# Optimization experiments

Hardware: AMD Instinct MI355X
Metric: run time of the kernel (lower is better)

Reference implementation:

```python
import jax, jax.numpy as jnp
import numpy as np

NUM_FRAMES = 32
H, W = 1024, 1024
MAX_DEPTH = 5
PROB_THRESHOLD = 1e-3  # torch skips children with topk prob <= 0.001


def setup_inputs() -> dict:
    key = jax.random.key(0)
    k1, k2 = jax.random.split(key)
    frame_colors = jax.random.uniform(k1, (NUM_FRAMES, 3), dtype=jnp.float32)
    # torch init: rand(num_frames, 2, num_frames) * 5
    frame_selection = jax.random.uniform(k2, (NUM_FRAMES, 2, NUM_FRAMES), dtype=jnp.float32) * 5.0
    return {"frame_colors": frame_colors, "frame_selection": frame_selection, "temperature": 1}


def _np_softmax(x):
    e = np.exp(x - x.max(axis=-1, keepdims=True))
    return e / e.sum(axis=-1, keepdims=True)


def _render(idx, depth, h, w, fc, fs_probs, probs_np, memo):
    # Output depends only on (idx, depth, h, w) since split_ratio is a constant
    # 0.5 buffer and split_direction = idx % 2, so identical subtrees are memoized.
    key = (idx, depth, h, w)
    if key in memo:
        return memo[key]
    if depth >= MAX_DEPTH or w < 2 or h < 2:
        out = jnp.broadcast_to(jax.nn.sigmoid(fc[idx]).reshape(3, 1, 1), (3, h, w))
    else:
        vertical = (idx % 2) == 1  # split_directions[i] = i % 2
        if vertical:
            lw = max(1, int(w * 0.5))
            child_sizes = ((h, lw), (h, w - lw))  # left cols [0:lw], right cols [lw:]
        else:
            th = max(1, int(h * 0.5))
            child_sizes = ((th, w), (h - th, w))  # top rows [0:th], bottom rows [th:]
        k = 3 if depth < 2 else (2 if depth < 4 else 1)
        k = min(k, NUM_FRAMES)
        parts = []
        for side in range(2):  # 0 = left/top, 1 = right/bottom
            ch, cw = child_sizes[side]
            pn = probs_np[idx, side]
            order = np.argsort(-pn)[:k]  # top-k child frame indices (constant w.r.t. grads)
            probs = fs_probs[idx, side]
            acc = jnp.zeros((3, ch, cw), dtype=fc.dtype)
            for i in order:
                if pn[i] > PROB_THRESHOLD:  # same skip rule as torch, decided on concrete values
                    child = _render(int(i), depth + 1, ch, cw, fc, fs_probs, probs_np, memo)
                    acc = acc + probs[i] * child
            parts.append(acc)
        out = jnp.concatenate(parts, axis=2 if vertical else 1)
    memo[key] = out
    return out


def reference(frame_colors, frame_selection, temperature):
    t = float(temperature)
    fs_probs = jax.nn.softmax(frame_selection / t, axis=-1)  # (F, 2, F) differentiable weights
    probs_np = _np_softmax(np.asarray(frame_selection, dtype=np.float64) / t)  # structure only
    return _render(0, 0, H, W, frame_colors, fs_probs, probs_np, {})
```

## Files before the change

### kernel.cpp

```cpp
#include <hip/hip_runtime.h>
#include <math.h>

#define NF 32
#define HH 1024
#define WW 1024

__device__ __forceinline__ int descend(int idx, int py, int px,
                                       int& y0, int& x0, int& h, int& w) {
  int side;
  if (idx & 1) {
    int lw = w >> 1;
    if (px >= x0 + lw) { side = 1; x0 += lw; w -= lw; }
    else               { side = 0; w = lw; }
  } else {
    int th = h >> 1;
    if (py >= y0 + th) { side = 1; y0 += th; h -= th; }
    else               { side = 0; h = th; }
  }
  return side;
}

__global__ __launch_bounds__(256)
void fractal_kernel(const float* __restrict__ fc,
                    const float* __restrict__ fsel,
                    const int* __restrict__ temp,
                    float* __restrict__ out) {
  __shared__ float sProbs[64][33];
  __shared__ int   sOrder[64][3];
  __shared__ float sSig[NF][3];
  __shared__ float sCol[3];

  const int tid  = threadIdx.x;
  const int tile = blockIdx.x;
  const int by = tile >> 5, bx = tile & 31;
  const int py = by * 32 + 16, px = bx * 32 + 16;

  int   ti = temp[0];
  float t  = (ti > 0 && ti < 1000000) ? (float)ti : __int_as_float(ti);
  const float invT = 1.0f / t;

  for (int v = 0; v < 8; ++v) {
    int u = v * 256 + tid;
    sProbs[u >> 5][u & 31] = fsel[u] * invT;
  }
  if (tid >= 64 && tid < 160) {
    int j = tid - 64;
    sSig[j / 3][j % 3] = 1.0f / (1.0f + expf(-fc[j]));
  }
  __syncthreads();

  if (tid < 64) {
    float m = -1e30f;
    for (int i = 0; i < 32; ++i) m = fmaxf(m, sProbs[tid][i]);
    float s = 0.f;
    for (int i = 0; i < 32; ++i) {
      float e = expf(sProbs[tid][i] - m);
      sProbs[tid][i] = e;
      s += e;
    }
    float inv = 1.0f / s;
    float v0 = -1.f, v1 = -1.f, v2 = -1.f;
    int   b0 = 0,    b1 = 0,    b2 = 0;
    for (int i = 0; i < 32; ++i) {
      float p = sProbs[tid][i] * inv;
      sProbs[tid][i] = p;
      if (p > v0)      { v2=v1;b2=b1; v1=v0;b1=b0; v0=p;b0=i; }
      else if (p > v1) { v2=v1;b2=b1; v1=p;b1=i; }
      else if (p > v2) { v2=p;b2=i; }
    }
    sOrder[tid][0] = b0; sOrder[tid][1] = b1; sOrder[tid][2] = b2;
  }
  __syncthreads();

  if (tid < 64) {
    float c0 = 0.f, c1 = 0.f, c2 = 0.f;
    if (tid < 36) {
      int j = tid;
      int sel0 = j / 12; int r = j % 12;
      int sel1 = r / 4;  r &= 3;
      int sel2 = r >> 1;
      int sel3 = r & 1;
      int selArr[5] = { sel0, sel1, sel2, sel3, 0 };

      int idx = 0, ay = 0, ax = 0, ah = HH, aw = WW;
      float w = 1.0f;
      bool alive = true;
      for (int d = 0; d < 5; ++d) {
        int s   = descend(idx, py, px, ay, ax, ah, aw);
        int row = idx * 2 + s;
        int ci  = sOrder[row][selArr[d]];
        float p = sProbs[row][ci];
        if (p <= 1e-3f) { alive = false; break; }
        w  *= p;
        idx = ci;
      }
      if (alive) {
        c0 = w * sSig[idx][0];
        c1 = w * sSig[idx][1];
        c2 = w * sSig[idx][2];
      }
    }
    for (int off = 32; off > 0; off >>= 1) {
      c0 += __shfl_down(c0, off, 64);
      c1 += __shfl_down(c1, off, 64);
      c2 += __shfl_down(c2, off, 64);
    }
    if (tid == 0) { sCol[0] = c0; sCol[1] = c1; sCol[2] = c2; }
  }
  __syncthreads();

  const int r = tid >> 3;
  const int q = tid & 7;
  for (int c = 0; c < 3; ++c) {
    float v = sCol[c];
    float4 val = make_float4(v, v, v, v);
    float* base = out + (size_t)c * (HH * WW)
                      + (size_t)(by * 32 + r) * WW + (size_t)bx * 32;
    ((float4*)base)[q] = val;
  }
}

extern "C" void kernel_launch(void* const* d_in, const int* in_sizes, int n_in,
                              void* d_out, int out_size, void* d_ws, size_t ws_size,
                              hipStream_t stream) {
  const float* fc   = (const float*)d_in[0];
  const float* fsel = (const float*)d_in[1];
  const int*   temp = (const int*)d_in[2];
  float* out = (float*)d_out;
  (void)in_sizes; (void)n_in; (void)out_size; (void)d_ws; (void)ws_size;
  fractal_kernel<<<dim3(1024), dim3(256), 0, stream>>>(fc, fsel, temp, out);
}
```

Measured before the change: 66.05 us.

## Split into tile-colour kernel and separate coalesced broadcast-write kernel

Before, each of the 1024 blocks recomputed the full softmax/top-k setup just to colour one 32x32 tile. Now a small 32-block kernel does that setup once per block and computes 32 tile colours (8 per wave), storing them in workspace. A second kernel writes the output with fully row-contiguous float4 stores. This removes most of the redundant setup work and improves the store pattern, at the cost of an extra launch and a workspace round trip.

```diff
diff --git a/kernel.cpp b/kernel.cpp
--- a/kernel.cpp
+++ b/kernel.cpp
@@ -4,6 +4,7 @@
 #define NF 32
 #define HH 1024
 #define WW 1024
+
 
 __device__ __forceinline__ int descend(int idx, int py, int px,
                                        int& y0, int& x0, int& h, int& w) {
@@ -21,19 +22,15 @@
 }
 
 __global__ __launch_bounds__(256)
-void fractal_kernel(const float* __restrict__ fc,
-                    const float* __restrict__ fsel,
-                    const int* __restrict__ temp,
-                    float* __restrict__ out) {
+void tiles_kernel(const float* __restrict__ fc,
+                  const float* __restrict__ fsel,
+                  const int* __restrict__ temp,
+                  float4* __restrict__ tileCol) {
   __shared__ float sProbs[64][33];
   __shared__ int   sOrder[64][3];
   __shared__ float sSig[NF][3];
-  __shared__ float sCol[3];
 
-  const int tid  = threadIdx.x;
-  const int tile = blockIdx.x;
-  const int by = tile >> 5, bx = tile & 31;
-  const int py = by * 32 + 16, px = bx * 32 + 16;
+  const int tid = threadIdx.x;
 
   int   ti = temp[0];
   float t  = (ti > 0 && ti < 1000000) ? (float)ti : __int_as_float(ti);
@@ -72,10 +69,16 @@
   }
   __syncthreads();
 
-  if (tid < 64) {
+  const int wave = tid >> 6;
+  const int lane = tid & 63;
+  for (int k = 0; k < 8; ++k) {
+    const int tile = blockIdx.x * 32 + wave * 8 + k;
+    const int py = ((tile >> 5) << 5) + 16;
+    const int px = ((tile & 31) << 5) + 16;
+
     float c0 = 0.f, c1 = 0.f, c2 = 0.f;
-    if (tid < 36) {
-      int j = tid;
+    if (lane < 36) {
+      int j = lane;
       int sel0 = j / 12; int r = j % 12;
       int sel1 = r / 4;  r &= 3;
       int sel2 = r >> 1;
@@ -105,19 +108,22 @@
       c1 += __shfl_down(c1, off, 64);
       c2 += __shfl_down(c2, off, 64);
     }
-    if (tid == 0) { sCol[0] = c0; sCol[1] = c1; sCol[2] = c2; }
+    if (lane == 0) tileCol[tile] = make_float4(c0, c1, c2, 0.f);
   }
-  __syncthreads();
+}
 
-  const int r = tid >> 3;
-  const int q = tid & 7;
-  for (int c = 0; c < 3; ++c) {
-    float v = sCol[c];
-    float4 val = make_float4(v, v, v, v);
-    float* base = out + (size_t)c * (HH * WW)
-                      + (size_t)(by * 32 + r) * WW + (size_t)bx * 32;
-    ((float4*)base)[q] = val;
-  }
+__global__ __launch_bounds__(256)
+void write_kernel(const float4* __restrict__ tileCol,
+                  float4* __restrict__ out4) {
+  const int g  = blockIdx.x * 256 + threadIdx.x;
+  const int y  = g >> 8;
+  const int xq = g & 255;
+  const int tile = ((y >> 5) << 5) + (xq >> 3);
+  const float4 col = tileCol[tile];
+
+  out4[g]                   = make_float4(col.x, col.x, col.x, col.x);
+  out4[g + (HH * WW / 4)]   = make_float4(col.y, col.y, col.y, col.y);
+  out4[g + (HH * WW / 2)]   = make_float4(col.z, col.z, col.z, col.z);
 }
 
 extern "C" void kernel_launch(void* const* d_in, const int* in_sizes, int n_in,
@@ -126,7 +132,9 @@
   const float* fc   = (const float*)d_in[0];
   const float* fsel = (const float*)d_in[1];
   const int*   temp = (const int*)d_in[2];
-  float* out = (float*)d_out;
-  (void)in_sizes; (void)n_in; (void)out_size; (void)d_ws; (void)ws_size;
-  fractal_kernel<<<dim3(1024), dim3(256), 0, stream>>>(fc, fsel, temp, out);
+  float4* tileCol = (float4*)d_ws;
+  (void)in_sizes; (void)n_in; (void)out_size; (void)ws_size;
+
+  tiles_kernel<<<dim3(32),   dim3(256), 0, stream>>>(fc, fsel, temp, tileCol);
+  write_kernel<<<dim3(1024), dim3(256), 0, stream>>>(tileCol, (float4*)d_out);
 }
```

Result: slower. 74.17 us (+12.3%).
